# Kernel optimization log

Hardware: AMD Instinct MI355X
Metric: run time of the kernel (lower is better)

Reference implementation:

```python
import jax, jax.numpy as jnp
import numpy as np

N_ZONE, E_ZONE = 100000, 2000000
N_OUT, E_OUT = 50000, 1000000
N_GND, E_GND = 50000, 1000000
HID = 64


def _gcn_conv(x, W, b, edge_index, edge_weight, num_nodes):
    """PyG GCNConv with normalize=True, add_self_loops=True (fill_value=1).
    out[i] = sum_{e: col[e]=i} d^-1/2[row]*w_e*d^-1/2[col] * (xW)[row[e]]
             + d^-1[i]*(xW)[i] + b
    """
    row, col = edge_index[0], edge_index[1]
    ew = edge_weight.reshape(-1)  # [E,1] -> [E]
    # degree includes self-loop weight of 1
    deg = jax.ops.segment_sum(ew, col, num_segments=num_nodes) + 1.0
    dinv = jnp.where(deg > 0, jax.lax.rsqrt(deg), 0.0)
    norm = dinv[row] * ew * dinv[col]  # [E]
    h = x @ W  # [N, HID] transform first (tiny in-dim)
    agg = jax.ops.segment_sum(norm[:, None] * h[row], col, num_segments=num_nodes)
    agg = agg + (dinv * dinv)[:, None] * h  # self-loop term
    return agg + b


def setup_inputs() -> dict:
    key = jax.random.key(0)
    ks = jax.random.split(key, 16)
    inp = {}
    inp["x_zone"] = jax.random.normal(ks[0], (N_ZONE, 2), dtype=jnp.float32)
    inp["x_outdoor"] = jax.random.normal(ks[1], (N_OUT, 3), dtype=jnp.float32)
    inp["x_ground"] = jax.random.normal(ks[2], (N_GND, 1), dtype=jnp.float32)
    inp["edge_index_zone"] = jax.random.randint(ks[3], (2, E_ZONE), 0, N_ZONE, dtype=jnp.int32)
    inp["edge_index_outdoor"] = jax.random.randint(ks[4], (2, E_OUT), 0, N_OUT, dtype=jnp.int32)
    inp["edge_index_ground"] = jax.random.randint(ks[5], (2, E_GND), 0, N_GND, dtype=jnp.int32)
    # learned params: GCN weights/biases + per-edge attribute parameters
    inp["W_zone"] = jax.random.normal(ks[6], (2, HID), dtype=jnp.float32) * 0.5
    inp["W_outdoor"] = jax.random.normal(ks[7], (3, HID), dtype=jnp.float32) * 0.5
    inp["W_ground"] = jax.random.normal(ks[8], (1, HID), dtype=jnp.float32) * 0.5
    inp["b_zone"] = jnp.zeros((HID,), dtype=jnp.float32)
    inp["b_outdoor"] = jnp.zeros((HID,), dtype=jnp.float32)
    inp["b_ground"] = jnp.zeros((HID,), dtype=jnp.float32)
    # positive edge weights so symmetric normalization deg^-1/2 is finite
    inp["edge_attr_zone"] = jax.random.uniform(ks[9], (E_ZONE, 1), dtype=jnp.float32, minval=0.1, maxval=1.0)
    inp["edge_attr_outdoor"] = jax.random.uniform(ks[10], (E_OUT, 1), dtype=jnp.float32, minval=0.1, maxval=1.0)
    inp["edge_attr_ground"] = jax.random.uniform(ks[11], (E_GND, 1), dtype=jnp.float32, minval=0.1, maxval=1.0)
    return inp


def reference(x_zone, x_outdoor, x_ground,
              edge_index_zone, edge_index_outdoor, edge_index_ground,
              W_zone, W_outdoor, W_ground,
              b_zone, b_outdoor, b_ground,
              edge_attr_zone, edge_attr_outdoor, edge_attr_ground):
    z = _gcn_conv(x_zone, W_zone, b_zone, edge_index_zone, edge_attr_zone, N_ZONE)
    o = _gcn_conv(x_outdoor, W_outdoor, b_outdoor, edge_index_outdoor, edge_attr_outdoor, N_OUT)
    g = _gcn_conv(x_ground, W_ground, b_ground, edge_index_ground, edge_attr_ground, N_GND)
    return (jax.nn.relu(z), jax.nn.relu(o), jax.nn.relu(g))
```

## Files before the change

kernel.cpp:

```cpp
#include <hip/hip_runtime.h>

#define N_ZONE 100000
#define E_ZONE 2000000
#define N_OUT  50000
#define E_OUT  1000000
#define N_GND  50000
#define E_GND  1000000
#define HID    64
#define N_TOT   (N_ZONE + N_OUT + N_GND)
#define E_TOTAL (E_ZONE + E_OUT + E_GND)

#define RANGE   2048
#define RSHIFT  11
#define NBZ     49
#define NBO     25
#define NBG     25
#define NBUCKET (NBZ + NBO + NBG)
#define SLICES  12
#define OUT_PAD_BASE (NBZ * RANGE)
#define GND_PAD_BASE ((NBZ + NBO) * RANGE)
#define PAD_TOT      (NBUCKET * RANGE)

#define WREC  0
#define WCTR  (2 * E_TOTAL)
#define WPART (WCTR + 384)
#define WPDEG WPART
#define WPSZ  WPART
#define WPSO  (WPSZ + NBZ * SLICES * RANGE * 2)
#define WPSG  (WPSO + NBO * SLICES * RANGE * 3)
#define WPEND (WPSG + NBG * SLICES * RANGE)
#define WDINV WPEND
#define WYZ   (WDINV + PAD_TOT)
#define WYO   (WYZ + 2 * N_ZONE)
#define WYG   (WYO + 4 * N_OUT)
#define WUZ   (WYG + N_GND)
#define WUO   (WUZ + 2 * N_ZONE)
#define WUG   (WUO + 4 * N_OUT)
#define WTOT  (WUG + N_GND)
#define FAST_WS_BYTES ((size_t)WTOT * 4)

#define CNT_CHUNK 16384
#define BIN_CHUNK 4096

__global__ void k_count(const int* __restrict__ eiz, const int* __restrict__ eio,
                        const int* __restrict__ eig, unsigned* __restrict__ cnt) {
    __shared__ unsigned hist[NBUCKET];
    int tid = threadIdx.x;
    for (int b = tid; b < NBUCKET; b += 256) hist[b] = 0;
    __syncthreads();
    int t0 = blockIdx.x * CNT_CHUNK;
#pragma unroll 4
    for (int i = 0; i < CNT_CHUNK / 256; i++) {
        int t = t0 + i * 256 + tid;
        if (t < E_TOTAL) {
            int b;
            if (t < E_ZONE) b = eiz[E_ZONE + t] >> RSHIFT;
            else if (t < E_ZONE + E_OUT) b = NBZ + (eio[E_OUT + (t - E_ZONE)] >> RSHIFT);
            else b = NBZ + NBO + (eig[E_GND + (t - E_ZONE - E_OUT)] >> RSHIFT);
            atomicAdd(&hist[b], 1u);
        }
    }
    __syncthreads();
    for (int b = tid; b < NBUCKET; b += 256)
        if (hist[b]) atomicAdd(&cnt[b], hist[b]);
}

__global__ void k_scan(unsigned* __restrict__ ctr) {
    if (threadIdx.x == 0) {
        unsigned acc = 0;
        for (int b = 0; b < NBUCKET; b++) {
            ctr[256 + b] = acc;
            ctr[128 + b] = acc;
            acc += ctr[b];
        }
    }
}

__global__ void k_bin(const int* __restrict__ eiz, const float* __restrict__ wz,
                      const int* __restrict__ eio, const float* __restrict__ wo,
                      const int* __restrict__ eig, const float* __restrict__ wg,
                      unsigned* __restrict__ ctr, uint2* __restrict__ rec) {
    __shared__ unsigned lds_a[BIN_CHUNK];
    __shared__ float    lds_w[BIN_CHUNK];
    __shared__ unsigned hist[NBUCKET];
    __shared__ unsigned sbase[NBUCKET];
    __shared__ unsigned gbase[NBUCKET];
    unsigned* cur = ctr + 128;
    int tid = threadIdx.x;
    for (int b = tid; b < NBUCKET; b += 256) hist[b] = 0;
    __syncthreads();
    int t0 = blockIdx.x * BIN_CHUNK;
    unsigned mya[BIN_CHUNK / 256], myb[BIN_CHUNK / 256], myr[BIN_CHUNK / 256];
    float myw[BIN_CHUNK / 256];
#pragma unroll
    for (int i = 0; i < BIN_CHUNK / 256; i++) {
        int t = t0 + i * 256 + tid;
        unsigned b = 0xFFFFFFFFu;
        if (t < E_TOTAL) {
            int row, col; float w;
            if (t < E_ZONE) { row = eiz[t]; col = eiz[E_ZONE + t]; w = wz[t]; b = col >> RSHIFT; }
            else if (t < E_ZONE + E_OUT) { int e = t - E_ZONE; row = eio[e]; col = eio[E_OUT + e]; w = wo[e]; b = NBZ + (col >> RSHIFT); }
            else { int e = t - E_ZONE - E_OUT; row = eig[e]; col = eig[E_GND + e]; w = wg[e]; b = NBZ + NBO + (col >> RSHIFT); }
            mya[i] = ((unsigned)(col & (RANGE - 1)) << 17) | (unsigned)row;
            myw[i] = w;
            myr[i] = atomicAdd(&hist[b], 1u);
        }
        myb[i] = b;
    }
    __syncthreads();
    if (tid == 0) {
        unsigned acc = 0;
        for (int b = 0; b < NBUCKET; b++) { sbase[b] = acc; acc += hist[b]; }
    }
    __syncthreads();
    for (int b = tid; b < NBUCKET; b += 256)
        gbase[b] = hist[b] ? atomicAdd(&cur[b], hist[b]) : 0u;
#pragma unroll
    for (int i = 0; i < BIN_CHUNK / 256; i++) {
        if (myb[i] < NBUCKET) {
            unsigned p = sbase[myb[i]] + myr[i];
            lds_a[p] = mya[i];
            lds_w[p] = myw[i];
        }
    }
    __syncthreads();
    int wid = tid >> 6, lane = tid & 63;
    for (int b = wid; b < NBUCKET; b += 4) {
        unsigned c = hist[b], gb = gbase[b], sb = sbase[b];
        for (unsigned j = lane; j < c; j += 64)
            rec[gb + j] = make_uint2(lds_a[sb + j], __float_as_uint(lds_w[sb + j]));
    }
}

__global__ void k_degp(const uint2* __restrict__ rec, const unsigned* __restrict__ ctr,
                       float* __restrict__ pdeg) {
    __shared__ float deg[RANGE];
    int r = blockIdx.x / SLICES, sl = blockIdx.x % SLICES, tid = threadIdx.x;
    for (int i = tid; i < RANGE; i += 256) deg[i] = 0.0f;
    __syncthreads();
    unsigned c = ctr[r], b0 = ctr[256 + r];
    unsigned per = (c + SLICES - 1) / SLICES;
    unsigned s0 = sl * per;
    unsigned s1 = s0 + per; if (s1 > c) s1 = c;
    for (unsigned j = s0 + tid; j < s1; j += 256) {
        uint2 q = rec[b0 + j];
        atomicAdd(&deg[q.x >> 17], __uint_as_float(q.y));
    }
    __syncthreads();
    float* o = pdeg + (size_t)blockIdx.x * RANGE;
    for (int i = tid * 4; i < RANGE; i += 1024) {
        float4 v = *(float4*)&deg[i];
        *(float4*)&o[i] = v;
    }
}

__global__ void k_dinvy(const float* __restrict__ xz, const float* __restrict__ xo,
                        const float* __restrict__ xg, float* __restrict__ ws) {
    int p = blockIdx.x * blockDim.x + threadIdx.x;
    if (p >= PAD_TOT) return;
    int r = p >> RSHIFT, i = p & (RANGE - 1);
    float d = 1.0f;
#pragma unroll
    for (int sl = 0; sl < SLICES; sl++)
        d += ws[WPDEG + (size_t)(r * SLICES + sl) * RANGE + i];
    float di = rsqrtf(d);
    ws[WDINV + p] = di;
    if (p < OUT_PAD_BASE) {
        if (p < N_ZONE) {
            ws[WYZ + 2 * p]     = di * xz[2 * p];
            ws[WYZ + 2 * p + 1] = di * xz[2 * p + 1];
        }
    } else if (p < GND_PAD_BASE) {
        int idx = p - OUT_PAD_BASE;
        if (idx < N_OUT) {
            ws[WYO + 4 * idx]     = di * xo[3 * idx];
            ws[WYO + 4 * idx + 1] = di * xo[3 * idx + 1];
            ws[WYO + 4 * idx + 2] = di * xo[3 * idx + 2];
            ws[WYO + 4 * idx + 3] = 0.0f;
        }
    } else {
        int idx = p - GND_PAD_BASE;
        if (idx < N_GND) ws[WYG + idx] = di * xg[idx];
    }
}

template<int CH, int RSTART, int YOFF, int PSOFF>
__global__ void k_spT(float* __restrict__ ws) {
    __shared__ __align__(16) float s[RANGE * CH];
    int r = blockIdx.x / SLICES, sl = blockIdx.x % SLICES, tid = threadIdx.x;
    const unsigned* ctr = (const unsigned*)(ws + WCTR);
    const uint2* rec = (const uint2*)ws;
    const int tot = RANGE * CH;
    for (int i = tid; i < tot; i += 256) s[i] = 0.0f;
    __syncthreads();
    int rb = RSTART + r;
    unsigned c = ctr[rb], b0 = ctr[256 + rb];
    unsigned per = (c + SLICES - 1) / SLICES;
    unsigned s0 = sl * per;
    unsigned s1 = s0 + per; if (s1 > c) s1 = c;
    if constexpr (CH == 2) {
        const float2* y = (const float2*)(ws + YOFF);
        for (unsigned j = s0 + tid; j < s1; j += 256) {
            uint2 q = rec[b0 + j];
            unsigned colr = q.x >> 17, row = q.x & 0x1FFFFu;
            float w = __uint_as_float(q.y);
            float2 yv = y[row];
            atomicAdd(&s[colr * 2],     w * yv.x);
            atomicAdd(&s[colr * 2 + 1], w * yv.y);
        }
    } else if constexpr (CH == 3) {
        const float4* y = (const float4*)(ws + YOFF);
        for (unsigned j = s0 + tid; j < s1; j += 256) {
            uint2 q = rec[b0 + j];
            unsigned colr = q.x >> 17, row = q.x & 0x1FFFFu;
            float w = __uint_as_float(q.y);
            float4 yv = y[row];
            atomicAdd(&s[colr * 3],     w * yv.x);
            atomicAdd(&s[colr * 3 + 1], w * yv.y);
            atomicAdd(&s[colr * 3 + 2], w * yv.z);
        }
    } else {
        const float* y = ws + YOFF;
        for (unsigned j = s0 + tid; j < s1; j += 256) {
            uint2 q = rec[b0 + j];
            atomicAdd(&s[q.x >> 17], __uint_as_float(q.y) * y[q.x & 0x1FFFFu]);
        }
    }
    __syncthreads();
    float* o = ws + PSOFF + (size_t)(r * SLICES + sl) * tot;
    for (int i = tid * 4; i < tot; i += 1024) {
        float4 v = *(float4*)&s[i];
        *(float4*)&o[i] = v;
    }
}

__global__ void k_u(float* __restrict__ ws) {
    int p = blockIdx.x * blockDim.x + threadIdx.x;
    if (p >= PAD_TOT) return;
    int r = p >> RSHIFT, i = p & (RANGE - 1);
    float di = ws[WDINV + p];
    if (p < OUT_PAD_BASE) {
        if (p >= N_ZONE) return;
        float s0 = ws[WYZ + 2 * p], s1 = ws[WYZ + 2 * p + 1];
#pragma unroll
        for (int sl = 0; sl < SLICES; sl++) {
            const float* ps = ws + WPSZ + (size_t)(r * SLICES + sl) * RANGE * 2;
            s0 += ps[2 * i]; s1 += ps[2 * i + 1];
        }
        ws[WUZ + 2 * p] = di * s0; ws[WUZ + 2 * p + 1] = di * s1;
    } else if (p < GND_PAD_BASE) {
        int idx = p - OUT_PAD_BASE;
        if (idx >= N_OUT) return;
        int rg = r - NBZ;
        float s0 = ws[WYO + 4 * idx], s1 = ws[WYO + 4 * idx + 1], s2 = ws[WYO + 4 * idx + 2];
#pragma unroll
        for (int sl = 0; sl < SLICES; sl++) {
            const float* ps = ws + WPSO + (size_t)(rg * SLICES + sl) * RANGE * 3;
            s0 += ps[3 * i]; s1 += ps[3 * i + 1]; s2 += ps[3 * i + 2];
        }
        ws[WUO + 4 * idx] = di * s0; ws[WUO + 4 * idx + 1] = di * s1; ws[WUO + 4 * idx + 2] = di * s2;
    } else {
        int idx = p - GND_PAD_BASE;
        if (idx >= N_GND) return;
        int rg = r - NBZ - NBO;
        float s0 = ws[WYG + idx];
#pragma unroll
        for (int sl = 0; sl < SLICES; sl++)
            s0 += ws[WPSG + (size_t)(rg * SLICES + sl) * RANGE + i];
        ws[WUG + idx] = di * s0;
    }
}

__global__ void k_fin2(const float* __restrict__ ws,
                       const float* __restrict__ Wz, const float* __restrict__ bz,
                       const float* __restrict__ Wo, const float* __restrict__ bo,
                       const float* __restrict__ Wg, const float* __restrict__ bg,
                       float* __restrict__ out) {
    int t = blockIdx.x * blockDim.x + threadIdx.x;
    const int TZ4 = N_ZONE * 16, TO4 = TZ4 + N_OUT * 16, TG4 = TO4 + N_GND * 16;
    if (t < TZ4) {
        int i = t >> 4, jb = (t & 15) << 2;
        float u0 = ws[WUZ + 2 * i], u1 = ws[WUZ + 2 * i + 1];
        float4 w0 = *(const float4*)(Wz + jb);
        float4 w1 = *(const float4*)(Wz + HID + jb);
        float4 bv = *(const float4*)(bz + jb);
        float4 o;
        o.x = fmaxf(bv.x + u0 * w0.x + u1 * w1.x, 0.0f);
        o.y = fmaxf(bv.y + u0 * w0.y + u1 * w1.y, 0.0f);
        o.z = fmaxf(bv.z + u0 * w0.z + u1 * w1.z, 0.0f);
        o.w = fmaxf(bv.w + u0 * w0.w + u1 * w1.w, 0.0f);
        *(float4*)(out + i * HID + jb) = o;
    } else if (t < TO4) {
        int q = t - TZ4;
        int i = q >> 4, jb = (q & 15) << 2;
        const float* u = ws + WUO + 4 * i;
        float u0 = u[0], u1 = u[1], u2 = u[2];
        float4 w0 = *(const float4*)(Wo + jb);
        float4 w1 = *(const float4*)(Wo + HID + jb);
        float4 w2 = *(const float4*)(Wo + 2 * HID + jb);
        float4 bv = *(const float4*)(bo + jb);
        float4 o;
        o.x = fmaxf(bv.x + u0 * w0.x + u1 * w1.x + u2 * w2.x, 0.0f);
        o.y = fmaxf(bv.y + u0 * w0.y + u1 * w1.y + u2 * w2.y, 0.0f);
        o.z = fmaxf(bv.z + u0 * w0.z + u1 * w1.z + u2 * w2.z, 0.0f);
        o.w = fmaxf(bv.w + u0 * w0.w + u1 * w1.w + u2 * w2.w, 0.0f);
        *(float4*)(out + N_ZONE * HID + i * HID + jb) = o;
    } else if (t < TG4) {
        int q = t - TO4;
        int i = q >> 4, jb = (q & 15) << 2;
        float u0 = ws[WUG + i];
        float4 w0 = *(const float4*)(Wg + jb);
        float4 bv = *(const float4*)(bg + jb);
        float4 o;
        o.x = fmaxf(bv.x + u0 * w0.x, 0.0f);
        o.y = fmaxf(bv.y + u0 * w0.y, 0.0f);
        o.z = fmaxf(bv.z + u0 * w0.z, 0.0f);
        o.w = fmaxf(bv.w + u0 * w0.w, 0.0f);
        *(float4*)(out + (N_ZONE + N_OUT) * HID + i * HID + jb) = o;
    }
}

#define F_DEG_Z   0
#define F_DEG_O   (N_ZONE)
#define F_DEG_G   (N_ZONE + N_OUT)
#define F_DEG_TOT N_TOT
#define F_S_Z     F_DEG_TOT
#define F_S_O     (F_S_Z + N_ZONE * 2)
#define F_S_G     (F_S_O + N_OUT * 3)
#define F_TOT     (F_S_G + N_GND * 1)

__global__ void f_init(float* __restrict__ ws) {
    int i = blockIdx.x * blockDim.x + threadIdx.x;
    if (i < F_TOT) ws[i] = (i < F_DEG_TOT) ? 1.0f : 0.0f;
}
__global__ void f_deg(const int* __restrict__ eiz, const float* __restrict__ wz,
                      const int* __restrict__ eio, const float* __restrict__ wo,
                      const int* __restrict__ eig, const float* __restrict__ wg,
                      float* __restrict__ ws) {
    int t = blockIdx.x * blockDim.x + threadIdx.x;
    if (t < E_ZONE) atomicAdd(ws + F_DEG_Z + eiz[E_ZONE + t], wz[t]);
    else if (t < E_ZONE + E_OUT) { int e = t - E_ZONE; atomicAdd(ws + F_DEG_O + eio[E_OUT + e], wo[e]); }
    else if (t < E_ZONE + E_OUT + E_GND) { int e = t - E_ZONE - E_OUT; atomicAdd(ws + F_DEG_G + eig[E_GND + e], wg[e]); }
}
__global__ void f_dinv(float* __restrict__ ws) {
    int i = blockIdx.x * blockDim.x + threadIdx.x;
    if (i < F_DEG_TOT) ws[i] = 1.0f / sqrtf(ws[i]);
}
__global__ void f_scatter(const int* __restrict__ eiz, const float* __restrict__ wz, const float* __restrict__ xz,
                          const int* __restrict__ eio, const float* __restrict__ wo, const float* __restrict__ xo,
                          const int* __restrict__ eig, const float* __restrict__ wg, const float* __restrict__ xg,
                          float* __restrict__ ws) {
    int t = blockIdx.x * blockDim.x + threadIdx.x;
    if (t < E_ZONE) {
        int row = eiz[t], col = eiz[E_ZONE + t];
        float n = ws[F_DEG_Z + row] * wz[t] * ws[F_DEG_Z + col];
        atomicAdd(ws + F_S_Z + col * 2 + 0, n * xz[row * 2 + 0]);
        atomicAdd(ws + F_S_Z + col * 2 + 1, n * xz[row * 2 + 1]);
    } else if (t < E_ZONE + E_OUT) {
        int e = t - E_ZONE;
        int row = eio[e], col = eio[E_OUT + e];
        float n = ws[F_DEG_O + row] * wo[e] * ws[F_DEG_O + col];
        atomicAdd(ws + F_S_O + col * 3 + 0, n * xo[row * 3 + 0]);
        atomicAdd(ws + F_S_O + col * 3 + 1, n * xo[row * 3 + 1]);
        atomicAdd(ws + F_S_O + col * 3 + 2, n * xo[row * 3 + 2]);
    } else if (t < E_ZONE + E_OUT + E_GND) {
        int e = t - E_ZONE - E_OUT;
        int row = eig[e], col = eig[E_GND + e];
        float n = ws[F_DEG_G + row] * wg[e] * ws[F_DEG_G + col];
        atomicAdd(ws + F_S_G + col, n * xg[row]);
    }
}
__global__ void f_final(const float* __restrict__ ws,
                        const float* __restrict__ xz, const float* __restrict__ Wz, const float* __restrict__ bz,
                        const float* __restrict__ xo, const float* __restrict__ Wo, const float* __restrict__ bo,
                        const float* __restrict__ xg, const float* __restrict__ Wg, const float* __restrict__ bg,
                        float* __restrict__ out) {
    int t = blockIdx.x * blockDim.x + threadIdx.x;
    const int TZ = N_ZONE * HID, TO = TZ + N_OUT * HID, TG = TO + N_GND * HID;
    if (t < TZ) {
        int i = t >> 6, j = t & 63;
        float di = ws[F_DEG_Z + i], d2 = di * di;
        float t0 = ws[F_S_Z + i * 2 + 0] + d2 * xz[i * 2 + 0];
        float t1 = ws[F_S_Z + i * 2 + 1] + d2 * xz[i * 2 + 1];
        out[t] = fmaxf(bz[j] + t0 * Wz[j] + t1 * Wz[HID + j], 0.0f);
    } else if (t < TO) {
        int u = t - TZ;
        int i = u >> 6, j = u & 63;
        float di = ws[F_DEG_O + i], d2 = di * di;
        float t0 = ws[F_S_O + i * 3 + 0] + d2 * xo[i * 3 + 0];
        float t1 = ws[F_S_O + i * 3 + 1] + d2 * xo[i * 3 + 1];
        float t2 = ws[F_S_O + i * 3 + 2] + d2 * xo[i * 3 + 2];
        out[t] = fmaxf(bo[j] + t0 * Wo[j] + t1 * Wo[HID + j] + t2 * Wo[2 * HID + j], 0.0f);
    } else if (t < TG) {
        int u = t - TO;
        int i = u >> 6, j = u & 63;
        float di = ws[F_DEG_G + i], d2 = di * di;
        float t0 = ws[F_S_G + i] + d2 * xg[i];
        out[t] = fmaxf(bg[j] + t0 * Wg[j], 0.0f);
    }
}

extern "C" void kernel_launch(void* const* d_in, const int* in_sizes, int n_in,
                              void* d_out, int out_size, void* d_ws, size_t ws_size,
                              hipStream_t stream) {
    const float* xz = (const float*)d_in[0];
    const float* xo = (const float*)d_in[1];
    const float* xg = (const float*)d_in[2];
    const int*  eiz = (const int*)d_in[3];
    const int*  eio = (const int*)d_in[4];
    const int*  eig = (const int*)d_in[5];
    const float* Wz = (const float*)d_in[6];
    const float* Wo = (const float*)d_in[7];
    const float* Wg = (const float*)d_in[8];
    const float* bz = (const float*)d_in[9];
    const float* bo = (const float*)d_in[10];
    const float* bg = (const float*)d_in[11];
    const float* wz = (const float*)d_in[12];
    const float* wo = (const float*)d_in[13];
    const float* wg = (const float*)d_in[14];
    float* out = (float*)d_out;
    float* ws  = (float*)d_ws;

    const int B = 256;

    if (ws_size >= FAST_WS_BYTES) {
        unsigned* ctr = (unsigned*)(ws + WCTR);
        uint2* rec = (uint2*)ws;
        hipMemsetAsync(ctr, 0, 384 * 4, stream);
        k_count<<<(E_TOTAL + CNT_CHUNK - 1) / CNT_CHUNK, B, 0, stream>>>(eiz, eio, eig, ctr);
        k_scan<<<1, 64, 0, stream>>>(ctr);
        k_bin<<<(E_TOTAL + BIN_CHUNK - 1) / BIN_CHUNK, B, 0, stream>>>(eiz, wz, eio, wo, eig, wg, ctr, rec);
        k_degp<<<NBUCKET * SLICES, B, 0, stream>>>(rec, ctr, ws + WPDEG);
        k_dinvy<<<(PAD_TOT + B - 1) / B, B, 0, stream>>>(xz, xo, xg, ws);
        k_spT<2, 0, WYZ, WPSZ><<<NBZ * SLICES, B, 0, stream>>>(ws);
        k_spT<3, NBZ, WYO, WPSO><<<NBO * SLICES, B, 0, stream>>>(ws);
        k_spT<1, NBZ + NBO, WYG, WPSG><<<NBG * SLICES, B, 0, stream>>>(ws);
        k_u<<<(PAD_TOT + B - 1) / B, B, 0, stream>>>(ws);
        k_fin2<<<(N_TOT * HID / 4 + B - 1) / B, B, 0, stream>>>(ws, Wz, bz, Wo, bo, Wg, bg, out);
    } else {
        const int E_TOT = E_TOTAL, OUT_TOT = N_TOT * HID;
        f_init<<<(F_TOT + B - 1) / B, B, 0, stream>>>(ws);
        f_deg<<<(E_TOT + B - 1) / B, B, 0, stream>>>(eiz, wz, eio, wo, eig, wg, ws);
        f_dinv<<<(F_DEG_TOT + B - 1) / B, B, 0, stream>>>(ws);
        f_scatter<<<(E_TOT + B - 1) / B, B, 0, stream>>>(eiz, wz, xz, eio, wo, xo, eig, wg, xg, ws);
        f_final<<<(OUT_TOT + B - 1) / B, B, 0, stream>>>(ws, xz, Wz, bz, xo, Wo, bo, xg, Wg, bg, out);
    }
}
```

Baseline: 301.4 us.

## Fuse GCN pipeline into one persistent kernel with software grid barriers

Replaces the chain of about ten kernel launches and a memset (count, scan, bin, degree partials, dinv, per-type sparse aggregation, reduce, final projection) with a single persistent kernel of 768 blocks. The stages are separated by atomic-counter grid barriers, and work is spread with grid-stride and task loops. This removes per-launch overhead and the idle tails between dependent kernels. It also drops slices per bucket from 12 to 8 and halves the binning chunk. The cost is that all blocks must be co-resident, spin-wait barriers add latency, and the reset of the magic-flag and counter can race across repeated calls.

```diff
diff --git a/kernel.cpp b/kernel.cpp
--- a/kernel.cpp
+++ b/kernel.cpp
@@ -16,307 +16,348 @@
 #define NBO     25
 #define NBG     25
 #define NBUCKET (NBZ + NBO + NBG)
-#define SLICES  12
+#define SLICES  8
+#define NTASK   (NBUCKET * SLICES)
 #define OUT_PAD_BASE (NBZ * RANGE)
 #define GND_PAD_BASE ((NBZ + NBO) * RANGE)
 #define PAD_TOT      (NBUCKET * RANGE)
 
-#define WREC  0
-#define WCTR  (2 * E_TOTAL)
-#define WPART (WCTR + 384)
-#define WPDEG WPART
-#define WPSZ  WPART
+#define GRID  768
+#define BLK   256
+#define CHUNK 2048
+#define NCHUNK ((E_TOTAL + CHUNK - 1) / CHUNK)
+
+#define WFLAG 0
+#define WBARC 16
+#define WCNT  64
+#define WBASE 192
+#define WCUR  320
+#define WREC  512
+#define WPDEG (WREC + 2 * E_TOTAL)
+#define WPSZ  (WPDEG + NTASK * RANGE)
 #define WPSO  (WPSZ + NBZ * SLICES * RANGE * 2)
 #define WPSG  (WPSO + NBO * SLICES * RANGE * 3)
-#define WPEND (WPSG + NBG * SLICES * RANGE)
-#define WDINV WPEND
-#define WYZ   (WDINV + PAD_TOT)
-#define WYO   (WYZ + 2 * N_ZONE)
+#define WDINV (WPSG + NBG * SLICES * RANGE)
+#define WY    (WDINV + PAD_TOT)
+#define WYZ   WY
+#define WYO   (WY + 2 * N_ZONE)
 #define WYG   (WYO + 4 * N_OUT)
-#define WUZ   (WYG + N_GND)
-#define WUO   (WUZ + 2 * N_ZONE)
+#define WU    (WY + 450000)
+#define WUZ   WU
+#define WUO   (WU + 2 * N_ZONE)
 #define WUG   (WUO + 4 * N_OUT)
-#define WTOT  (WUG + N_GND)
+#define WTOT  (WU + 450000)
 #define FAST_WS_BYTES ((size_t)WTOT * 4)
 
-#define CNT_CHUNK 16384
-#define BIN_CHUNK 4096
-
-__global__ void k_count(const int* __restrict__ eiz, const int* __restrict__ eio,
-                        const int* __restrict__ eig, unsigned* __restrict__ cnt) {
-    __shared__ unsigned hist[NBUCKET];
-    int tid = threadIdx.x;
-    for (int b = tid; b < NBUCKET; b += 256) hist[b] = 0;
+#define MAGIC 0x5EED5EEDu
+
+__device__ __forceinline__ void gbar(unsigned* ctr, unsigned target) {
     __syncthreads();
-    int t0 = blockIdx.x * CNT_CHUNK;
-#pragma unroll 4
-    for (int i = 0; i < CNT_CHUNK / 256; i++) {
-        int t = t0 + i * 256 + tid;
-        if (t < E_TOTAL) {
-            int b;
-            if (t < E_ZONE) b = eiz[E_ZONE + t] >> RSHIFT;
-            else if (t < E_ZONE + E_OUT) b = NBZ + (eio[E_OUT + (t - E_ZONE)] >> RSHIFT);
-            else b = NBZ + NBO + (eig[E_GND + (t - E_ZONE - E_OUT)] >> RSHIFT);
-            atomicAdd(&hist[b], 1u);
-        }
+    if (threadIdx.x == 0) {
+        __threadfence();
+        __hip_atomic_fetch_add(ctr, 1u, __ATOMIC_ACQ_REL, __HIP_MEMORY_SCOPE_AGENT);
+        while (__hip_atomic_load(ctr, __ATOMIC_ACQUIRE, __HIP_MEMORY_SCOPE_AGENT) < target)
+            __builtin_amdgcn_s_sleep(64);
+        __threadfence();
     }
     __syncthreads();
-    for (int b = tid; b < NBUCKET; b += 256)
-        if (hist[b]) atomicAdd(&cnt[b], hist[b]);
-}
-
-__global__ void k_scan(unsigned* __restrict__ ctr) {
-    if (threadIdx.x == 0) {
-        unsigned acc = 0;
-        for (int b = 0; b < NBUCKET; b++) {
-            ctr[256 + b] = acc;
-            ctr[128 + b] = acc;
-            acc += ctr[b];
-        }
-    }
-}
-
-__global__ void k_bin(const int* __restrict__ eiz, const float* __restrict__ wz,
-                      const int* __restrict__ eio, const float* __restrict__ wo,
-                      const int* __restrict__ eig, const float* __restrict__ wg,
-                      unsigned* __restrict__ ctr, uint2* __restrict__ rec) {
-    __shared__ unsigned lds_a[BIN_CHUNK];
-    __shared__ float    lds_w[BIN_CHUNK];
-    __shared__ unsigned hist[NBUCKET];
-    __shared__ unsigned sbase[NBUCKET];
-    __shared__ unsigned gbase[NBUCKET];
-    unsigned* cur = ctr + 128;
-    int tid = threadIdx.x;
-    for (int b = tid; b < NBUCKET; b += 256) hist[b] = 0;
+}
+
+__global__ __launch_bounds__(BLK, 4)
+void mega(const int* __restrict__ eiz, const float* __restrict__ wz,
+          const int* __restrict__ eio, const float* __restrict__ wo,
+          const int* __restrict__ eig, const float* __restrict__ wg,
+          const float* __restrict__ xz, const float* __restrict__ xo,
+          const float* __restrict__ xg,
+          const float* __restrict__ Wz, const float* __restrict__ bz,
+          const float* __restrict__ Wo, const float* __restrict__ bo,
+          const float* __restrict__ Wg, const float* __restrict__ bg,
+          float* __restrict__ out, float* __restrict__ ws) {
+    __shared__ __align__(16) float smem[RANGE * 3];
+    __shared__ unsigned hist[NBUCKET], sbase[NBUCKET], gbase[NBUCKET];
+
+    unsigned* uws = (unsigned*)ws;
+    unsigned* ctr = uws + WBARC;
+    const int tid = threadIdx.x;
+    const int bid = blockIdx.x;
+    const int nb  = gridDim.x;
+    const int gstride = nb * BLK;
+    uint2* rec = (uint2*)(ws + WREC);
+
+    if (bid == 0) {
+        if (tid < NBUCKET)
+            __hip_atomic_store(&uws[WCNT + tid], 0u, __ATOMIC_RELAXED, __HIP_MEMORY_SCOPE_AGENT);
+        __syncthreads();
+        if (tid == 0) {
+            __hip_atomic_store(ctr, 0u, __ATOMIC_RELAXED, __HIP_MEMORY_SCOPE_AGENT);
+            __threadfence();
+            __hip_atomic_store(&uws[WFLAG], MAGIC, __ATOMIC_RELEASE, __HIP_MEMORY_SCOPE_AGENT);
+        }
+    }
+    if (tid == 0) {
+        while (__hip_atomic_load(&uws[WFLAG], __ATOMIC_ACQUIRE, __HIP_MEMORY_SCOPE_AGENT) != MAGIC)
+            __builtin_amdgcn_s_sleep(32);
+        __threadfence();
+    }
     __syncthreads();
-    int t0 = blockIdx.x * BIN_CHUNK;
-    unsigned mya[BIN_CHUNK / 256], myb[BIN_CHUNK / 256], myr[BIN_CHUNK / 256];
-    float myw[BIN_CHUNK / 256];
-#pragma unroll
-    for (int i = 0; i < BIN_CHUNK / 256; i++) {
-        int t = t0 + i * 256 + tid;
-        unsigned b = 0xFFFFFFFFu;
-        if (t < E_TOTAL) {
-            int row, col; float w;
-            if (t < E_ZONE) { row = eiz[t]; col = eiz[E_ZONE + t]; w = wz[t]; b = col >> RSHIFT; }
-            else if (t < E_ZONE + E_OUT) { int e = t - E_ZONE; row = eio[e]; col = eio[E_OUT + e]; w = wo[e]; b = NBZ + (col >> RSHIFT); }
-            else { int e = t - E_ZONE - E_OUT; row = eig[e]; col = eig[E_GND + e]; w = wg[e]; b = NBZ + NBO + (col >> RSHIFT); }
-            mya[i] = ((unsigned)(col & (RANGE - 1)) << 17) | (unsigned)row;
-            myw[i] = w;
-            myr[i] = atomicAdd(&hist[b], 1u);
-        }
-        myb[i] = b;
-    }
+
+    for (int b = tid; b < NBUCKET; b += BLK) hist[b] = 0;
     __syncthreads();
-    if (tid == 0) {
-        unsigned acc = 0;
-        for (int b = 0; b < NBUCKET; b++) { sbase[b] = acc; acc += hist[b]; }
+    for (int t = bid * BLK + tid; t < E_TOTAL; t += gstride) {
+        int b;
+        if (t < E_ZONE) b = eiz[E_ZONE + t] >> RSHIFT;
+        else if (t < E_ZONE + E_OUT) b = NBZ + (eio[E_OUT + (t - E_ZONE)] >> RSHIFT);
+        else b = NBZ + NBO + (eig[E_GND + (t - E_ZONE - E_OUT)] >> RSHIFT);
+        atomicAdd(&hist[b], 1u);
     }
     __syncthreads();
-    for (int b = tid; b < NBUCKET; b += 256)
-        gbase[b] = hist[b] ? atomicAdd(&cur[b], hist[b]) : 0u;
-#pragma unroll
-    for (int i = 0; i < BIN_CHUNK / 256; i++) {
-        if (myb[i] < NBUCKET) {
-            unsigned p = sbase[myb[i]] + myr[i];
-            lds_a[p] = mya[i];
-            lds_w[p] = myw[i];
-        }
-    }
-    __syncthreads();
-    int wid = tid >> 6, lane = tid & 63;
-    for (int b = wid; b < NBUCKET; b += 4) {
-        unsigned c = hist[b], gb = gbase[b], sb = sbase[b];
-        for (unsigned j = lane; j < c; j += 64)
-            rec[gb + j] = make_uint2(lds_a[sb + j], __float_as_uint(lds_w[sb + j]));
-    }
-}
-
-__global__ void k_degp(const uint2* __restrict__ rec, const unsigned* __restrict__ ctr,
-                       float* __restrict__ pdeg) {
-    __shared__ float deg[RANGE];
-    int r = blockIdx.x / SLICES, sl = blockIdx.x % SLICES, tid = threadIdx.x;
-    for (int i = tid; i < RANGE; i += 256) deg[i] = 0.0f;
-    __syncthreads();
-    unsigned c = ctr[r], b0 = ctr[256 + r];
-    unsigned per = (c + SLICES - 1) / SLICES;
-    unsigned s0 = sl * per;
-    unsigned s1 = s0 + per; if (s1 > c) s1 = c;
-    for (unsigned j = s0 + tid; j < s1; j += 256) {
-        uint2 q = rec[b0 + j];
-        atomicAdd(&deg[q.x >> 17], __uint_as_float(q.y));
-    }
-    __syncthreads();
-    float* o = pdeg + (size_t)blockIdx.x * RANGE;
-    for (int i = tid * 4; i < RANGE; i += 1024) {
-        float4 v = *(float4*)&deg[i];
-        *(float4*)&o[i] = v;
-    }
-}
-
-__global__ void k_dinvy(const float* __restrict__ xz, const float* __restrict__ xo,
-                        const float* __restrict__ xg, float* __restrict__ ws) {
-    int p = blockIdx.x * blockDim.x + threadIdx.x;
-    if (p >= PAD_TOT) return;
-    int r = p >> RSHIFT, i = p & (RANGE - 1);
-    float d = 1.0f;
-#pragma unroll
-    for (int sl = 0; sl < SLICES; sl++)
-        d += ws[WPDEG + (size_t)(r * SLICES + sl) * RANGE + i];
-    float di = rsqrtf(d);
-    ws[WDINV + p] = di;
-    if (p < OUT_PAD_BASE) {
-        if (p < N_ZONE) {
-            ws[WYZ + 2 * p]     = di * xz[2 * p];
-            ws[WYZ + 2 * p + 1] = di * xz[2 * p + 1];
-        }
-    } else if (p < GND_PAD_BASE) {
-        int idx = p - OUT_PAD_BASE;
-        if (idx < N_OUT) {
-            ws[WYO + 4 * idx]     = di * xo[3 * idx];
-            ws[WYO + 4 * idx + 1] = di * xo[3 * idx + 1];
-            ws[WYO + 4 * idx + 2] = di * xo[3 * idx + 2];
-            ws[WYO + 4 * idx + 3] = 0.0f;
-        }
-    } else {
-        int idx = p - GND_PAD_BASE;
-        if (idx < N_GND) ws[WYG + idx] = di * xg[idx];
-    }
-}
-
-template<int CH, int RSTART, int YOFF, int PSOFF>
-__global__ void k_spT(float* __restrict__ ws) {
-    __shared__ __align__(16) float s[RANGE * CH];
-    int r = blockIdx.x / SLICES, sl = blockIdx.x % SLICES, tid = threadIdx.x;
-    const unsigned* ctr = (const unsigned*)(ws + WCTR);
-    const uint2* rec = (const uint2*)ws;
-    const int tot = RANGE * CH;
-    for (int i = tid; i < tot; i += 256) s[i] = 0.0f;
-    __syncthreads();
-    int rb = RSTART + r;
-    unsigned c = ctr[rb], b0 = ctr[256 + rb];
-    unsigned per = (c + SLICES - 1) / SLICES;
-    unsigned s0 = sl * per;
-    unsigned s1 = s0 + per; if (s1 > c) s1 = c;
-    if constexpr (CH == 2) {
-        const float2* y = (const float2*)(ws + YOFF);
-        for (unsigned j = s0 + tid; j < s1; j += 256) {
+    for (int b = tid; b < NBUCKET; b += BLK)
+        if (hist[b]) atomicAdd(&uws[WCNT + b], hist[b]);
+    gbar(ctr, 1u * nb);
+
+    if (bid == 0) {
+        if (tid < NBUCKET)
+            hist[tid] = __hip_atomic_load(&uws[WCNT + tid], __ATOMIC_RELAXED, __HIP_MEMORY_SCOPE_AGENT);
+        __syncthreads();
+        if (tid == 0) {
+            unsigned acc = 0;
+            for (int b = 0; b < NBUCKET; b++) { unsigned c = hist[b]; hist[b] = acc; acc += c; }
+        }
+        __syncthreads();
+        if (tid < NBUCKET) {
+            __hip_atomic_store(&uws[WBASE + tid], hist[tid], __ATOMIC_RELAXED, __HIP_MEMORY_SCOPE_AGENT);
+            __hip_atomic_store(&uws[WCUR + tid],  hist[tid], __ATOMIC_RELAXED, __HIP_MEMORY_SCOPE_AGENT);
+        }
+    }
+    gbar(ctr, 2u * nb);
+
+    {
+        unsigned* la = (unsigned*)smem;
+        float*    lw = smem + CHUNK;
+        for (int c = bid; c < NCHUNK; c += nb) {
+            for (int b = tid; b < NBUCKET; b += BLK) hist[b] = 0;
+            __syncthreads();
+            unsigned mya[CHUNK / BLK], mybk[CHUNK / BLK], myr[CHUNK / BLK];
+            float myw[CHUNK / BLK];
+            int t0 = c * CHUNK;
+#pragma unroll
+            for (int i = 0; i < CHUNK / BLK; i++) {
+                int t = t0 + i * BLK + tid;
+                unsigned b = 0xFFFFFFFFu;
+                if (t < E_TOTAL) {
+                    int row, col; float w;
+                    if (t < E_ZONE) { row = eiz[t]; col = eiz[E_ZONE + t]; w = wz[t]; b = col >> RSHIFT; }
+                    else if (t < E_ZONE + E_OUT) { int e = t - E_ZONE; row = eio[e]; col = eio[E_OUT + e]; w = wo[e]; b = NBZ + (col >> RSHIFT); }
+                    else { int e = t - E_ZONE - E_OUT; row = eig[e]; col = eig[E_GND + e]; w = wg[e]; b = NBZ + NBO + (col >> RSHIFT); }
+                    mya[i] = ((unsigned)(col & (RANGE - 1)) << 17) | (unsigned)row;
+                    myw[i] = w;
+                    myr[i] = atomicAdd(&hist[b], 1u);
+                }
+                mybk[i] = b;
+            }
+            __syncthreads();
+            if (tid == 0) {
+                unsigned acc = 0;
+                for (int b = 0; b < NBUCKET; b++) { sbase[b] = acc; acc += hist[b]; }
+            }
+            __syncthreads();
+            for (int b = tid; b < NBUCKET; b += BLK)
+                gbase[b] = hist[b] ? atomicAdd(&uws[WCUR + b], hist[b]) : 0u;
+            __syncthreads();
+#pragma unroll
+            for (int i = 0; i < CHUNK / BLK; i++) {
+                if (mybk[i] < NBUCKET) {
+                    unsigned p = sbase[mybk[i]] + myr[i];
+                    la[p] = mya[i]; lw[p] = myw[i];
+                }
+            }
+            __syncthreads();
+            int wid = tid >> 6, lane = tid & 63;
+            for (int b = wid; b < NBUCKET; b += 4) {
+                unsigned cc = hist[b], gb = gbase[b], sb = sbase[b];
+                for (unsigned j = lane; j < cc; j += 64)
+                    rec[gb + j] = make_uint2(la[sb + j], __float_as_uint(lw[sb + j]));
+            }
+            __syncthreads();
+        }
+    }
+    gbar(ctr, 3u * nb);
+
+    for (int task = bid; task < NTASK; task += nb) {
+        int r = task / SLICES, sl = task % SLICES;
+        for (int i = tid; i < RANGE; i += BLK) smem[i] = 0.0f;
+        __syncthreads();
+        unsigned c = uws[WCNT + r], b0 = uws[WBASE + r];
+        unsigned per = (c + SLICES - 1) / SLICES;
+        unsigned s0 = sl * per, s1 = s0 + per; if (s1 > c) s1 = c;
+        for (unsigned j = s0 + tid; j < s1; j += BLK) {
             uint2 q = rec[b0 + j];
-            unsigned colr = q.x >> 17, row = q.x & 0x1FFFFu;
-            float w = __uint_as_float(q.y);
-            float2 yv = y[row];
-            atomicAdd(&s[colr * 2],     w * yv.x);
-            atomicAdd(&s[colr * 2 + 1], w * yv.y);
-        }
-    } else if constexpr (CH == 3) {
-        const float4* y = (const float4*)(ws + YOFF);
-        for (unsigned j = s0 + tid; j < s1; j += 256) {
-            uint2 q = rec[b0 + j];
-            unsigned colr = q.x >> 17, row = q.x & 0x1FFFFu;
-            float w = __uint_as_float(q.y);
-            float4 yv = y[row];
-            atomicAdd(&s[colr * 3],     w * yv.x);
-            atomicAdd(&s[colr * 3 + 1], w * yv.y);
-            atomicAdd(&s[colr * 3 + 2], w * yv.z);
-        }
-    } else {
-        const float* y = ws + YOFF;
-        for (unsigned j = s0 + tid; j < s1; j += 256) {
-            uint2 q = rec[b0 + j];
-            atomicAdd(&s[q.x >> 17], __uint_as_float(q.y) * y[q.x & 0x1FFFFu]);
-        }
-    }
-    __syncthreads();
-    float* o = ws + PSOFF + (size_t)(r * SLICES + sl) * tot;
-    for (int i = tid * 4; i < tot; i += 1024) {
-        float4 v = *(float4*)&s[i];
-        *(float4*)&o[i] = v;
-    }
-}
-
-__global__ void k_u(float* __restrict__ ws) {
-    int p = blockIdx.x * blockDim.x + threadIdx.x;
-    if (p >= PAD_TOT) return;
-    int r = p >> RSHIFT, i = p & (RANGE - 1);
-    float di = ws[WDINV + p];
-    if (p < OUT_PAD_BASE) {
-        if (p >= N_ZONE) return;
-        float s0 = ws[WYZ + 2 * p], s1 = ws[WYZ + 2 * p + 1];
-#pragma unroll
-        for (int sl = 0; sl < SLICES; sl++) {
-            const float* ps = ws + WPSZ + (size_t)(r * SLICES + sl) * RANGE * 2;
-            s0 += ps[2 * i]; s1 += ps[2 * i + 1];
-        }
-        ws[WUZ + 2 * p] = di * s0; ws[WUZ + 2 * p + 1] = di * s1;
-    } else if (p < GND_PAD_BASE) {
-        int idx = p - OUT_PAD_BASE;
-        if (idx >= N_OUT) return;
-        int rg = r - NBZ;
-        float s0 = ws[WYO + 4 * idx], s1 = ws[WYO + 4 * idx + 1], s2 = ws[WYO + 4 * idx + 2];
-#pragma unroll
-        for (int sl = 0; sl < SLICES; sl++) {
-            const float* ps = ws + WPSO + (size_t)(rg * SLICES + sl) * RANGE * 3;
-            s0 += ps[3 * i]; s1 += ps[3 * i + 1]; s2 += ps[3 * i + 2];
-        }
-        ws[WUO + 4 * idx] = di * s0; ws[WUO + 4 * idx + 1] = di * s1; ws[WUO + 4 * idx + 2] = di * s2;
-    } else {
-        int idx = p - GND_PAD_BASE;
-        if (idx >= N_GND) return;
-        int rg = r - NBZ - NBO;
-        float s0 = ws[WYG + idx];
+            atomicAdd(&smem[q.x >> 17], __uint_as_float(q.y));
+        }
+        __syncthreads();
+        float* o = ws + WPDEG + (size_t)task * RANGE;
+        for (int i = tid * 4; i < RANGE; i += BLK * 4)
+            *(float4*)&o[i] = *(float4*)&smem[i];
+        __syncthreads();
+    }
+    gbar(ctr, 4u * nb);
+
+    for (int p = bid * BLK + tid; p < PAD_TOT; p += gstride) {
+        int r = p >> RSHIFT, i = p & (RANGE - 1);
+        float d = 1.0f;
 #pragma unroll
         for (int sl = 0; sl < SLICES; sl++)
-            s0 += ws[WPSG + (size_t)(rg * SLICES + sl) * RANGE + i];
-        ws[WUG + idx] = di * s0;
-    }
-}
-
-__global__ void k_fin2(const float* __restrict__ ws,
-                       const float* __restrict__ Wz, const float* __restrict__ bz,
-                       const float* __restrict__ Wo, const float* __restrict__ bo,
-                       const float* __restrict__ Wg, const float* __restrict__ bg,
-                       float* __restrict__ out) {
-    int t = blockIdx.x * blockDim.x + threadIdx.x;
-    const int TZ4 = N_ZONE * 16, TO4 = TZ4 + N_OUT * 16, TG4 = TO4 + N_GND * 16;
-    if (t < TZ4) {
-        int i = t >> 4, jb = (t & 15) << 2;
-        float u0 = ws[WUZ + 2 * i], u1 = ws[WUZ + 2 * i + 1];
-        float4 w0 = *(const float4*)(Wz + jb);
-        float4 w1 = *(const float4*)(Wz + HID + jb);
-        float4 bv = *(const float4*)(bz + jb);
-        float4 o;
-        o.x = fmaxf(bv.x + u0 * w0.x + u1 * w1.x, 0.0f);
-        o.y = fmaxf(bv.y + u0 * w0.y + u1 * w1.y, 0.0f);
-        o.z = fmaxf(bv.z + u0 * w0.z + u1 * w1.z, 0.0f);
-        o.w = fmaxf(bv.w + u0 * w0.w + u1 * w1.w, 0.0f);
-        *(float4*)(out + i * HID + jb) = o;
-    } else if (t < TO4) {
-        int q = t - TZ4;
-        int i = q >> 4, jb = (q & 15) << 2;
-        const float* u = ws + WUO + 4 * i;
-        float u0 = u[0], u1 = u[1], u2 = u[2];
-        float4 w0 = *(const float4*)(Wo + jb);
-        float4 w1 = *(const float4*)(Wo + HID + jb);
-        float4 w2 = *(const float4*)(Wo + 2 * HID + jb);
-        float4 bv = *(const float4*)(bo + jb);
-        float4 o;
-        o.x = fmaxf(bv.x + u0 * w0.x + u1 * w1.x + u2 * w2.x, 0.0f);
-        o.y = fmaxf(bv.y + u0 * w0.y + u1 * w1.y + u2 * w2.y, 0.0f);
-        o.z = fmaxf(bv.z + u0 * w0.z + u1 * w1.z + u2 * w2.z, 0.0f);
-        o.w = fmaxf(bv.w + u0 * w0.w + u1 * w1.w + u2 * w2.w, 0.0f);
-        *(float4*)(out + N_ZONE * HID + i * HID + jb) = o;
-    } else if (t < TG4) {
-        int q = t - TO4;
-        int i = q >> 4, jb = (q & 15) << 2;
-        float u0 = ws[WUG + i];
-        float4 w0 = *(const float4*)(Wg + jb);
-        float4 bv = *(const float4*)(bg + jb);
-        float4 o;
-        o.x = fmaxf(bv.x + u0 * w0.x, 0.0f);
-        o.y = fmaxf(bv.y + u0 * w0.y, 0.0f);
-        o.z = fmaxf(bv.z + u0 * w0.z, 0.0f);
-        o.w = fmaxf(bv.w + u0 * w0.w, 0.0f);
-        *(float4*)(out + (N_ZONE + N_OUT) * HID + i * HID + jb) = o;
+            d += ws[WPDEG + (size_t)(r * SLICES + sl) * RANGE + i];
+        float di = rsqrtf(d);
+        ws[WDINV + p] = di;
+        if (p < OUT_PAD_BASE) {
+            if (p < N_ZONE) {
+                ws[WYZ + 2 * p]     = di * xz[2 * p];
+                ws[WYZ + 2 * p + 1] = di * xz[2 * p + 1];
+            }
+        } else if (p < GND_PAD_BASE) {
+            int idx = p - OUT_PAD_BASE;
+            if (idx < N_OUT) {
+                ws[WYO + 4 * idx]     = di * xo[3 * idx];
+                ws[WYO + 4 * idx + 1] = di * xo[3 * idx + 1];
+                ws[WYO + 4 * idx + 2] = di * xo[3 * idx + 2];
+                ws[WYO + 4 * idx + 3] = 0.0f;
+            }
+        } else {
+            int idx = p - GND_PAD_BASE;
+            if (idx < N_GND) ws[WYG + idx] = di * xg[idx];
+        }
+    }
+    gbar(ctr, 5u * nb);
+
+    for (int task = bid; task < NTASK; task += nb) {
+        int r = task / SLICES, sl = task % SLICES;
+        int ch, rg; size_t yoff, psoff;
+        if (r < NBZ)            { ch = 2; rg = r;             yoff = WYZ; psoff = WPSZ; }
+        else if (r < NBZ + NBO) { ch = 3; rg = r - NBZ;       yoff = WYO; psoff = WPSO; }
+        else                    { ch = 1; rg = r - NBZ - NBO; yoff = WYG; psoff = WPSG; }
+        int tot = RANGE * ch;
+        for (int i = tid; i < tot; i += BLK) smem[i] = 0.0f;
+        __syncthreads();
+        unsigned c = uws[WCNT + r], b0 = uws[WBASE + r];
+        unsigned per = (c + SLICES - 1) / SLICES;
+        unsigned s0 = sl * per, s1 = s0 + per; if (s1 > c) s1 = c;
+        if (ch == 2) {
+            const float2* y = (const float2*)(ws + yoff);
+            for (unsigned j = s0 + tid; j < s1; j += BLK) {
+                uint2 q = rec[b0 + j];
+                unsigned colr = q.x >> 17, row = q.x & 0x1FFFFu;
+                float w = __uint_as_float(q.y);
+                float2 yv = y[row];
+                atomicAdd(&smem[colr * 2],     w * yv.x);
+                atomicAdd(&smem[colr * 2 + 1], w * yv.y);
+            }
+        } else if (ch == 3) {
+            const float4* y = (const float4*)(ws + yoff);
+            for (unsigned j = s0 + tid; j < s1; j += BLK) {
+                uint2 q = rec[b0 + j];
+                unsigned colr = q.x >> 17, row = q.x & 0x1FFFFu;
+                float w = __uint_as_float(q.y);
+                float4 yv = y[row];
+                atomicAdd(&smem[colr * 3],     w * yv.x);
+                atomicAdd(&smem[colr * 3 + 1], w * yv.y);
+                atomicAdd(&smem[colr * 3 + 2], w * yv.z);
+            }
+        } else {
+            const float* y = ws + yoff;
+            for (unsigned j = s0 + tid; j < s1; j += BLK) {
+                uint2 q = rec[b0 + j];
+                atomicAdd(&smem[q.x >> 17], __uint_as_float(q.y) * y[q.x & 0x1FFFFu]);
+            }
+        }
+        __syncthreads();
+        float* o = ws + psoff + (size_t)(rg * SLICES + sl) * tot;
+        for (int i = tid * 4; i < tot; i += BLK * 4)
+            *(float4*)&o[i] = *(float4*)&smem[i];
+        __syncthreads();
+    }
+    gbar(ctr, 6u * nb);
+
+    for (int p = bid * BLK + tid; p < PAD_TOT; p += gstride) {
+        int r = p >> RSHIFT, i = p & (RANGE - 1);
+        float di = ws[WDINV + p];
+        if (p < OUT_PAD_BASE) {
+            if (p >= N_ZONE) continue;
+            float s0 = ws[WYZ + 2 * p], s1 = ws[WYZ + 2 * p + 1];
+#pragma unroll
+            for (int sl = 0; sl < SLICES; sl++) {
+                const float* ps = ws + WPSZ + (size_t)(r * SLICES + sl) * RANGE * 2;
+                s0 += ps[2 * i]; s1 += ps[2 * i + 1];
+            }
+            ws[WUZ + 2 * p] = di * s0; ws[WUZ + 2 * p + 1] = di * s1;
+        } else if (p < GND_PAD_BASE) {
+            int idx = p - OUT_PAD_BASE;
+            if (idx >= N_OUT) continue;
+            int rg = r - NBZ;
+            float s0 = ws[WYO + 4 * idx], s1 = ws[WYO + 4 * idx + 1], s2 = ws[WYO + 4 * idx + 2];
+#pragma unroll
+            for (int sl = 0; sl < SLICES; sl++) {
+                const float* ps = ws + WPSO + (size_t)(rg * SLICES + sl) * RANGE * 3;
+                s0 += ps[3 * i]; s1 += ps[3 * i + 1]; s2 += ps[3 * i + 2];
+            }
+            ws[WUO + 4 * idx] = di * s0; ws[WUO + 4 * idx + 1] = di * s1; ws[WUO + 4 * idx + 2] = di * s2;
+        } else {
+            int idx = p - GND_PAD_BASE;
+            if (idx >= N_GND) continue;
+            int rg = r - NBZ - NBO;
+            float s0 = ws[WYG + idx];
+#pragma unroll
+            for (int sl = 0; sl < SLICES; sl++)
+                s0 += ws[WPSG + (size_t)(rg * SLICES + sl) * RANGE + i];
+            ws[WUG + idx] = di * s0;
+        }
+    }
+    gbar(ctr, 7u * nb);
+
+    {
+        const int TZ4 = N_ZONE * 16, TO4 = TZ4 + N_OUT * 16, TG4 = TO4 + N_GND * 16;
+        for (int t = bid * BLK + tid; t < TG4; t += gstride) {
+            if (t < TZ4) {
+                int i = t >> 4, jb = (t & 15) << 2;
+                float u0 = ws[WUZ + 2 * i], u1 = ws[WUZ + 2 * i + 1];
+                float4 w0 = *(const float4*)(Wz + jb);
+                float4 w1 = *(const float4*)(Wz + HID + jb);
+                float4 bv = *(const float4*)(bz + jb);
+                float4 o;
+                o.x = fmaxf(bv.x + u0 * w0.x + u1 * w1.x, 0.0f);
+                o.y = fmaxf(bv.y + u0 * w0.y + u1 * w1.y, 0.0f);
+                o.z = fmaxf(bv.z + u0 * w0.z + u1 * w1.z, 0.0f);
+                o.w = fmaxf(bv.w + u0 * w0.w + u1 * w1.w, 0.0f);
+                *(float4*)(out + i * HID + jb) = o;
+            } else if (t < TO4) {
+                int q = t - TZ4;
+                int i = q >> 4, jb = (q & 15) << 2;
+                const float* u = ws + WUO + 4 * i;
+                float u0 = u[0], u1 = u[1], u2 = u[2];
+                float4 w0 = *(const float4*)(Wo + jb);
+                float4 w1 = *(const float4*)(Wo + HID + jb);
+                float4 w2 = *(const float4*)(Wo + 2 * HID + jb);
+                float4 bv = *(const float4*)(bo + jb);
+                float4 o;
+                o.x = fmaxf(bv.x + u0 * w0.x + u1 * w1.x + u2 * w2.x, 0.0f);
+                o.y = fmaxf(bv.y + u0 * w0.y + u1 * w1.y + u2 * w2.y, 0.0f);
+                o.z = fmaxf(bv.z + u0 * w0.z + u1 * w1.z + u2 * w2.z, 0.0f);
+                o.w = fmaxf(bv.w + u0 * w0.w + u1 * w1.w + u2 * w2.w, 0.0f);
+                *(float4*)(out + N_ZONE * HID + i * HID + jb) = o;
+            } else {
+                int q = t - TO4;
+                int i = q >> 4, jb = (q & 15) << 2;
+                float u0 = ws[WUG + i];
+                float4 w0 = *(const float4*)(Wg + jb);
+                float4 bv = *(const float4*)(bg + jb);
+                float4 o;
+                o.x = fmaxf(bv.x + u0 * w0.x, 0.0f);
+                o.y = fmaxf(bv.y + u0 * w0.y, 0.0f);
+                o.z = fmaxf(bv.z + u0 * w0.z, 0.0f);
+                o.w = fmaxf(bv.w + u0 * w0.w, 0.0f);
+                *(float4*)(out + (N_ZONE + N_OUT) * HID + i * HID + jb) = o;
+            }
+        }
     }
 }
 
@@ -424,19 +465,8 @@
     const int B = 256;
 
     if (ws_size >= FAST_WS_BYTES) {
-        unsigned* ctr = (unsigned*)(ws + WCTR);
-        uint2* rec = (uint2*)ws;
-        hipMemsetAsync(ctr, 0, 384 * 4, stream);
-        k_count<<<(E_TOTAL + CNT_CHUNK - 1) / CNT_CHUNK, B, 0, stream>>>(eiz, eio, eig, ctr);
-        k_scan<<<1, 64, 0, stream>>>(ctr);
-        k_bin<<<(E_TOTAL + BIN_CHUNK - 1) / BIN_CHUNK, B, 0, stream>>>(eiz, wz, eio, wo, eig, wg, ctr, rec);
-        k_degp<<<NBUCKET * SLICES, B, 0, stream>>>(rec, ctr, ws + WPDEG);
-        k_dinvy<<<(PAD_TOT + B - 1) / B, B, 0, stream>>>(xz, xo, xg, ws);
-        k_spT<2, 0, WYZ, WPSZ><<<NBZ * SLICES, B, 0, stream>>>(ws);
-        k_spT<3, NBZ, WYO, WPSO><<<NBO * SLICES, B, 0, stream>>>(ws);
-        k_spT<1, NBZ + NBO, WYG, WPSG><<<NBG * SLICES, B, 0, stream>>>(ws);
-        k_u<<<(PAD_TOT + B - 1) / B, B, 0, stream>>>(ws);
-        k_fin2<<<(N_TOT * HID / 4 + B - 1) / B, B, 0, stream>>>(ws, Wz, bz, Wo, bo, Wg, bg, out);
+        mega<<<GRID, BLK, 0, stream>>>(eiz, wz, eio, wo, eig, wg,
+                                       xz, xo, xg, Wz, bz, Wo, bo, Wg, bg, out, ws);
     } else {
         const int E_TOT = E_TOTAL, OUT_TOT = N_TOT * HID;
         f_init<<<(F_TOT + B - 1) / B, B, 0, stream>>>(ws);
```

New measurement: 1.033 ms. 3.43x slower.
